# Performance work log

Hardware: AMD Instinct MI355X
Metric: run time of the kernel (lower is better)

## Reference

```python
import jax, jax.numpy as jnp
import numpy as np

N_USERS = 200000
N_ITEMS = 100000
N_NODES = N_USERS + N_ITEMS
EMBED_DIM = 64
N_LAYERS = 3
N_EDGES = 5000000
BATCH = 4096


def setup_inputs() -> dict:
    key = jax.random.key(0)
    ks = jax.random.split(key, 8)
    # Xavier-uniform-ish init for embedding tables
    lim = float(np.sqrt(6.0 / (N_USERS + EMBED_DIM)))
    user_emb = jax.random.uniform(ks[0], (N_USERS, EMBED_DIM), jnp.float32, -lim, lim)
    lim_i = float(np.sqrt(6.0 / (N_ITEMS + EMBED_DIM)))
    item_emb = jax.random.uniform(ks[1], (N_ITEMS, EMBED_DIM), jnp.float32, -lim_i, lim_i)
    # sparse normalized adjacency in COO form (values ~ 1/sqrt(du*di), use small positives)
    adj_vals = jax.random.uniform(ks[2], (N_EDGES,), jnp.float32, 0.0, 0.1)
    adj_rows = jax.random.randint(ks[3], (N_EDGES,), 0, N_NODES, jnp.int32)
    adj_cols = jax.random.randint(ks[4], (N_EDGES,), 0, N_NODES, jnp.int32)
    users = jax.random.randint(ks[5], (BATCH,), 0, N_USERS, jnp.int32)
    pos_items = jax.random.randint(ks[6], (BATCH,), 0, N_ITEMS, jnp.int32)
    neg_items = jax.random.randint(ks[7], (BATCH,), 0, N_ITEMS, jnp.int32)
    return {
        "user_emb": user_emb, "item_emb": item_emb, "adj_vals": adj_vals,
        "adj_rows": adj_rows, "adj_cols": adj_cols,
        "users": users, "pos_items": pos_items, "neg_items": neg_items,
    }


def _spmm(adj_rows, adj_cols, adj_vals, x):
    # y = A @ x for sparse COO A: gather source rows, scale, scatter-add to dest rows
    msgs = adj_vals[:, None] * x[adj_cols]          # [n_edges, d]
    return jax.ops.segment_sum(msgs, adj_rows, num_segments=N_NODES)


def reference(user_emb, item_emb, adj_vals, adj_rows, adj_cols, users, pos_items, neg_items):
    # E^0 = concat(user, item); E^k = A @ E^{k-1}; final = mean over k=0..K
    E = jnp.concatenate([user_emb, item_emb], axis=0)   # [N_NODES, d]
    acc = E
    cur = E
    for _ in range(N_LAYERS):
        cur = _spmm(adj_rows, adj_cols, adj_vals, cur)
        acc = acc + cur
    E_final = acc / jnp.asarray(N_LAYERS + 1, E.dtype)
    e_u = E_final[users]                         # users index into user block
    e_pos = E_final[N_USERS + pos_items]         # items offset by n_users
    e_neg = E_final[N_USERS + neg_items]
    return jnp.stack([e_u, e_pos, e_neg], axis=0)  # [3, B, d]
```

## Files before the change

kernel.cpp:

```cpp
#include <hip/hip_runtime.h>
#include <hip/hip_fp16.h>
#include <stdint.h>

#define N_USERS   200000
#define N_ITEMS   100000
#define N_NODES   300000
#define EMBED_DIM 64
#define N_EDGES   5000000
#define BATCH     4096

#define ROWS_PER_BUCKET 512
#define PART_K 586
#define PART_B 1024
#define CHUNK  ((N_EDGES + PART_B - 1) / PART_B)
#define PART_L (PART_K * PART_B)
#define SCAN_T 1024
#define SCAN_NB (PART_L / SCAN_T)

#define VAL_SCALE 81920.0f
#define VAL_INV   (1.0f / 81920.0f)
#define FIN_CAP   10240

__global__ void part_count(const int* __restrict__ rows, int* __restrict__ hist) {
    __shared__ int h[PART_K];
    for (int i = threadIdx.x; i < PART_K; i += blockDim.x) h[i] = 0;
    __syncthreads();
    int beg = blockIdx.x * CHUNK;
    int end = min(beg + CHUNK, N_EDGES);
    for (int i = beg + (int)threadIdx.x; i < end; i += blockDim.x)
        atomicAdd(&h[rows[i] >> 9], 1);
    __syncthreads();
    for (int i = threadIdx.x; i < PART_K; i += blockDim.x)
        hist[blockIdx.x * PART_K + i] = h[i];
}

__global__ void scan_partial(const int* __restrict__ hist,
                             int* __restrict__ local_scan,
                             int* __restrict__ block_sums) {
    __shared__ int sh[SCAN_T];
    int tid = threadIdx.x;
    int gid = blockIdx.x * SCAN_T + tid;
    int b = gid & (PART_B - 1);
    int k = gid >> 10;
    int v = hist[b * PART_K + k];
    sh[tid] = v;
    __syncthreads();
    for (int off = 1; off < SCAN_T; off <<= 1) {
        int t = (tid >= off) ? sh[tid - off] : 0;
        __syncthreads();
        sh[tid] += t;
        __syncthreads();
    }
    local_scan[gid] = sh[tid] - v;
    if (tid == SCAN_T - 1) block_sums[blockIdx.x] = sh[tid];
}

__global__ void scan_blocksums(int* __restrict__ block_sums) {
    __shared__ int sh[1024];
    int tid = threadIdx.x;
    int v = (tid < SCAN_NB) ? block_sums[tid] : 0;
    sh[tid] = v;
    __syncthreads();
    for (int off = 1; off < 1024; off <<= 1) {
        int t = (tid >= off) ? sh[tid - off] : 0;
        __syncthreads();
        sh[tid] += t;
        __syncthreads();
    }
    if (tid < SCAN_NB) block_sums[tid] = sh[tid] - v;
}

__global__ void scan_addoff(const int* __restrict__ local_scan,
                            const int* __restrict__ block_sums,
                            int* __restrict__ sofs,
                            int* __restrict__ row_ptr) {
    int gid = blockIdx.x * SCAN_T + threadIdx.x;
    sofs[gid] = local_scan[gid] + block_sums[blockIdx.x];
    if (gid == 0) row_ptr[N_NODES] = N_EDGES;
}

__global__ void part_scatter(const int* __restrict__ rows,
                             const int* __restrict__ cols,
                             const float* __restrict__ vals,
                             const int* __restrict__ sofs,
                             int2* __restrict__ part) {
    __shared__ int lcnt[PART_K];
    __shared__ int lbase[PART_K];
    __shared__ int gbase[PART_K];
    __shared__ int sc[1024];
    __shared__ int2 buf[CHUNK];
    __shared__ unsigned short bkt[CHUNK];
    int b = blockIdx.x;
    int tid = threadIdx.x;
    for (int i = tid; i < PART_K; i += 1024) {
        lcnt[i] = 0;
        gbase[i] = sofs[i * PART_B + b];
    }
    __syncthreads();
    int beg = b * CHUNK;
    int end = min(beg + CHUNK, N_EDGES);
    int n = end - beg;
    for (int i = beg + tid; i < end; i += 1024)
        atomicAdd(&lcnt[rows[i] >> 9], 1);
    __syncthreads();
    int v = (tid < PART_K) ? lcnt[tid] : 0;
    sc[tid] = v;
    __syncthreads();
    for (int off = 1; off < 1024; off <<= 1) {
        int t = (tid >= off) ? sc[tid - off] : 0;
        __syncthreads();
        sc[tid] += t;
        __syncthreads();
    }
    if (tid < PART_K) {
        int excl = sc[tid] - v;
        lbase[tid] = excl;
        lcnt[tid] = excl;
    }
    __syncthreads();
    for (int i = beg + tid; i < end; i += 1024) {
        int r = rows[i];
        int k = r >> 9;
        int p = atomicAdd(&lcnt[k], 1);
        buf[p] = make_int2(cols[i] | ((r & 511) << 19), __float_as_int(vals[i]));
        bkt[p] = (unsigned short)k;
    }
    __syncthreads();
    for (int i = tid; i < n; i += 1024) {
        int k = bkt[i];
        part[gbase[k] + (i - lbase[k])] = buf[i];
    }
}

__global__ void csr_finalize(const int2* __restrict__ part,
                             const int* __restrict__ sofs,
                             int* __restrict__ row_ptr,
                             unsigned int* __restrict__ sorted) {
    __shared__ int cnt[ROWS_PER_BUCKET];
    __shared__ int cur[ROWS_PER_BUCKET];
    __shared__ int sc[ROWS_PER_BUCKET];
    __shared__ unsigned int obuf[FIN_CAP];
    int k = blockIdx.x;
    int tid = threadIdx.x;
    int seg_beg = sofs[k * PART_B];
    int seg_end = (k + 1 < PART_K) ? sofs[(k + 1) * PART_B] : N_EDGES;
    int n = seg_end - seg_beg;

    cnt[tid] = 0;
    __syncthreads();
    for (int i = seg_beg + tid; i < seg_end; i += ROWS_PER_BUCKET)
        atomicAdd(&cnt[(part[i].x >> 19) & 511], 1);
    __syncthreads();

    int v = cnt[tid];
    sc[tid] = v;
    __syncthreads();
    for (int off = 1; off < 512; off <<= 1) {
        int t = (tid >= off) ? sc[tid - off] : 0;
        __syncthreads();
        sc[tid] += t;
        __syncthreads();
    }
    int excl = sc[tid] - v;

    int row = k * ROWS_PER_BUCKET + tid;
    if (row < N_NODES) row_ptr[row] = seg_beg + excl;
    cur[tid] = excl;
    __syncthreads();

    if (n <= FIN_CAP) {
        for (int i = seg_beg + tid; i < seg_end; i += ROWS_PER_BUCKET) {
            int2 p = part[i];
            int r = (p.x >> 19) & 511;
            int lp = atomicAdd(&cur[r], 1);
            float fv = __int_as_float(p.y);
            unsigned int q = (unsigned int)min(8191, (int)(fv * VAL_SCALE + 0.5f));
            obuf[lp] = (unsigned int)(p.x & 0x7FFFF) | (q << 19);
        }
        __syncthreads();
        for (int i = tid; i < n; i += ROWS_PER_BUCKET)
            sorted[seg_beg + i] = obuf[i];
    } else {
        for (int i = seg_beg + tid; i < seg_end; i += ROWS_PER_BUCKET) {
            int2 p = part[i];
            int r = (p.x >> 19) & 511;
            int lp = atomicAdd(&cur[r], 1);
            float fv = __int_as_float(p.y);
            unsigned int q = (unsigned int)min(8191, (int)(fv * VAL_SCALE + 0.5f));
            sorted[seg_beg + lp] = (unsigned int)(p.x & 0x7FFFF) | (q << 19);
        }
    }
}

__global__ void convert_emb(const float* __restrict__ ue,
                            const float* __restrict__ ie,
                            __half* __restrict__ xh) {
    int t = blockIdx.x * blockDim.x + threadIdx.x;
    if (t >= N_NODES * 16) return;
    int flat = t * 4;
    int row = flat >> 6;
    int off = flat & 63;
    const float* src = (row < N_USERS) ? (ue + (size_t)row * 64 + off)
                                       : (ie + (size_t)(row - N_USERS) * 64 + off);
    float4 v = *(const float4*)src;
    __half2 h0 = __floats2half2_rn(v.x, v.y);
    __half2 h1 = __floats2half2_rn(v.z, v.w);
    float2 packed;
    ((__half2*)&packed)[0] = h0;
    ((__half2*)&packed)[1] = h1;
    ((float2*)xh)[t] = packed;
}

#define ACC8(vv, r) { \
    const __half2* hp_ = (const __half2*)&(r); \
    float2 f0_ = __half22float2(hp_[0]); \
    float2 f1_ = __half22float2(hp_[1]); \
    float2 f2_ = __half22float2(hp_[2]); \
    float2 f3_ = __half22float2(hp_[3]); \
    acc[0] += (vv) * f0_.x; acc[1] += (vv) * f0_.y; \
    acc[2] += (vv) * f1_.x; acc[3] += (vv) * f1_.y; \
    acc[4] += (vv) * f2_.x; acc[5] += (vv) * f2_.y; \
    acc[6] += (vv) * f3_.x; acc[7] += (vv) * f3_.y; }

__global__ void spmm_h(const int* __restrict__ row_ptr,
                       const unsigned int* __restrict__ sorted,
                       const __half* __restrict__ xh,
                       __half* __restrict__ yh) {
    int t = blockIdx.x * blockDim.x + threadIdx.x;
    int row = t >> 3;
    int l8 = t & 7;
    if (row >= N_NODES) return;
    const float4* xv = (const float4*)xh;
    int beg = row_ptr[row];
    int end = row_ptr[row + 1];
    float acc[8] = {0.f, 0.f, 0.f, 0.f, 0.f, 0.f, 0.f, 0.f};
    int e = beg;
    for (; e + 2 <= end; e += 2) {
        unsigned int cv0 = sorted[e];
        unsigned int cv1 = sorted[e + 1];
        float4 r0 = xv[(size_t)(cv0 & 0x7FFFF) * 8 + l8];
        float4 r1 = xv[(size_t)(cv1 & 0x7FFFF) * 8 + l8];
        float v0 = (float)(cv0 >> 19) * VAL_INV;
        float v1 = (float)(cv1 >> 19) * VAL_INV;
        ACC8(v0, r0);
        ACC8(v1, r1);
    }
    if (e < end) {
        unsigned int cv = sorted[e];
        float4 r0 = xv[(size_t)(cv & 0x7FFFF) * 8 + l8];
        float v = (float)(cv >> 19) * VAL_INV;
        ACC8(v, r0);
    }
    float4 ov;
    ((__half2*)&ov)[0] = __floats2half2_rn(acc[0], acc[1]);
    ((__half2*)&ov)[1] = __floats2half2_rn(acc[2], acc[3]);
    ((__half2*)&ov)[2] = __floats2half2_rn(acc[4], acc[5]);
    ((__half2*)&ov)[3] = __floats2half2_rn(acc[6], acc[7]);
    ((float4*)yh)[(size_t)row * 8 + l8] = ov;
}

__global__ void final_kernel(const int* __restrict__ row_ptr,
                             const unsigned int* __restrict__ sorted,
                             const float* __restrict__ user_emb,
                             const float* __restrict__ item_emb,
                             const __half* __restrict__ E1h,
                             const __half* __restrict__ E2h,
                             const int* __restrict__ users,
                             const int* __restrict__ pos_items,
                             const int* __restrict__ neg_items,
                             float* __restrict__ out) {
    int t = blockIdx.x * blockDim.x + threadIdx.x;
    int slot = t >> 3;
    int l8 = t & 7;
    if (slot >= 3 * BATCH) return;
    int which = slot >> 12;
    int idx   = slot & (BATCH - 1);
    int node;
    if (which == 0)      node = users[idx];
    else if (which == 1) node = N_USERS + pos_items[idx];
    else                 node = N_USERS + neg_items[idx];

    const float4* e2v = (const float4*)E2h;

    float acc[8] = {0.f, 0.f, 0.f, 0.f, 0.f, 0.f, 0.f, 0.f};
    int beg = row_ptr[node];
    int end = row_ptr[node + 1];
    int e = beg;
    for (; e + 2 <= end; e += 2) {
        unsigned int cv0 = sorted[e];
        unsigned int cv1 = sorted[e + 1];
        float4 r0 = e2v[(size_t)(cv0 & 0x7FFFF) * 8 + l8];
        float4 r1 = e2v[(size_t)(cv1 & 0x7FFFF) * 8 + l8];
        float v0 = (float)(cv0 >> 19) * VAL_INV;
        float v1 = (float)(cv1 >> 19) * VAL_INV;
        ACC8(v0, r0);
        ACC8(v1, r1);
    }
    if (e < end) {
        unsigned int cv = sorted[e];
        float4 r0 = e2v[(size_t)(cv & 0x7FFFF) * 8 + l8];
        float v = (float)(cv >> 19) * VAL_INV;
        ACC8(v, r0);
    }

    const float* t0 = (node < N_USERS) ? (user_emb + (size_t)node * 64)
                                       : (item_emb + (size_t)(node - N_USERS) * 64);
    float4 e0a = ((const float4*)t0)[l8 * 2];
    float4 e0b = ((const float4*)t0)[l8 * 2 + 1];

    float4 e1c = ((const float4*)E1h)[(size_t)node * 8 + l8];
    float4 e2c = ((const float4*)E2h)[(size_t)node * 8 + l8];
    const __half2* h1 = (const __half2*)&e1c;
    const __half2* h2 = (const __half2*)&e2c;
    float e1[8], e2[8];
    {
        float2 a0 = __half22float2(h1[0]), a1 = __half22float2(h1[1]);
        float2 a2 = __half22float2(h1[2]), a3 = __half22float2(h1[3]);
        e1[0]=a0.x; e1[1]=a0.y; e1[2]=a1.x; e1[3]=a1.y;
        e1[4]=a2.x; e1[5]=a2.y; e1[6]=a3.x; e1[7]=a3.y;
        float2 b0 = __half22float2(h2[0]), b1 = __half22float2(h2[1]);
        float2 b2 = __half22float2(h2[2]), b3 = __half22float2(h2[3]);
        e2[0]=b0.x; e2[1]=b0.y; e2[2]=b1.x; e2[3]=b1.y;
        e2[4]=b2.x; e2[5]=b2.y; e2[6]=b3.x; e2[7]=b3.y;
    }
    float4 ra, rb;
    ra.x = (e0a.x + e1[0] + e2[0] + acc[0]) * 0.25f;
    ra.y = (e0a.y + e1[1] + e2[1] + acc[1]) * 0.25f;
    ra.z = (e0a.z + e1[2] + e2[2] + acc[2]) * 0.25f;
    ra.w = (e0a.w + e1[3] + e2[3] + acc[3]) * 0.25f;
    rb.x = (e0b.x + e1[4] + e2[4] + acc[4]) * 0.25f;
    rb.y = (e0b.y + e1[5] + e2[5] + acc[5]) * 0.25f;
    rb.z = (e0b.z + e1[6] + e2[6] + acc[6]) * 0.25f;
    rb.w = (e0b.w + e1[7] + e2[7] + acc[7]) * 0.25f;
    ((float4*)out)[(size_t)slot * 16 + l8 * 2]     = ra;
    ((float4*)out)[(size_t)slot * 16 + l8 * 2 + 1] = rb;
}

extern "C" void kernel_launch(void* const* d_in, const int* in_sizes, int n_in,
                              void* d_out, int out_size, void* d_ws, size_t ws_size,
                              hipStream_t stream) {
    const float* user_emb  = (const float*)d_in[0];
    const float* item_emb  = (const float*)d_in[1];
    const float* adj_vals  = (const float*)d_in[2];
    const int*   adj_rows  = (const int*)d_in[3];
    const int*   adj_cols  = (const int*)d_in[4];
    const int*   users     = (const int*)d_in[5];
    const int*   pos_items = (const int*)d_in[6];
    const int*   neg_items = (const int*)d_in[7];
    float* out = (float*)d_out;

    char* ws = (char*)d_ws;
    size_t off = 0;
    auto alloc = [&](size_t bytes) -> void* {
        void* p = ws + off;
        off = (off + bytes + 255) & ~(size_t)255;
        return p;
    };
    int*  hist       = (int*) alloc((size_t)(PART_L + 32) * sizeof(int));
    int*  local_scan = (int*) alloc((size_t)(PART_L + 32) * sizeof(int));
    int*  sofs       = (int*) alloc((size_t)(PART_L + 32) * sizeof(int));
    int*  block_sums = (int*) alloc((size_t)(SCAN_NB + 32) * sizeof(int));
    int*  row_ptr    = (int*) alloc((size_t)(N_NODES + 32) * sizeof(int));
    int2* part    = (int2*)alloc((size_t)N_EDGES * sizeof(int2));
    unsigned int* sorted = (unsigned int*)alloc((size_t)N_EDGES * sizeof(unsigned int));
    __half* x0h   = (__half*)alloc((size_t)N_NODES * EMBED_DIM * sizeof(__half));
    __half* E1h   = (__half*)alloc((size_t)N_NODES * EMBED_DIM * sizeof(__half));
    __half* E2h   = (__half*)alloc((size_t)N_NODES * EMBED_DIM * sizeof(__half));

    part_count<<<PART_B, 1024, 0, stream>>>(adj_rows, hist);
    scan_partial<<<SCAN_NB, SCAN_T, 0, stream>>>(hist, local_scan, block_sums);
    scan_blocksums<<<1, 1024, 0, stream>>>(block_sums);
    scan_addoff<<<SCAN_NB, SCAN_T, 0, stream>>>(local_scan, block_sums, sofs, row_ptr);
    part_scatter<<<PART_B, 1024, 0, stream>>>(adj_rows, adj_cols, adj_vals, sofs, part);
    csr_finalize<<<PART_K, ROWS_PER_BUCKET, 0, stream>>>(part, sofs, row_ptr, sorted);

    const int TB = 256;
    convert_emb<<<(N_NODES * 16 + TB - 1) / TB, TB, 0, stream>>>(user_emb, item_emb, x0h);

    int spmm_blocks = (N_NODES * 8 + TB - 1) / TB;
    spmm_h<<<spmm_blocks, TB, 0, stream>>>(row_ptr, sorted, x0h, E1h);
    spmm_h<<<spmm_blocks, TB, 0, stream>>>(row_ptr, sorted, E1h, E2h);

    int final_blocks = (3 * BATCH * 8 + TB - 1) / TB;
    final_kernel<<<final_blocks, TB, 0, stream>>>(
        row_ptr, sorted, user_emb, item_emb, E1h, E2h, users, pos_items, neg_items, out);
}
```

Baseline: 436.0 us.

## Vectorize partition loads, split payload/row arrays, swizzle chunk order, unroll SpMM by four

Edge-partition kernels now read rows, cols and vals as 128-bit vectors with a chunk size that is a multiple of four. Value quantization moves into the scatter kernel, and the 8-byte intermediate splits into a 4-byte payload plus a 2-byte local-row array, which cuts traffic into csr_finalize. Block-to-chunk order is swizzled in the scan and the scatter, changing which global offsets each block writes. The SpMM inner loop is unrolled to four gathers per iteration for more memory-level parallelism. The swizzle must stay consistent between part_count indexing and the scan mapping, or the CSR layout goes wrong.

```diff
diff --git a/kernel.cpp b/kernel.cpp
--- a/kernel.cpp
+++ b/kernel.cpp
@@ -12,7 +12,7 @@
 #define ROWS_PER_BUCKET 512
 #define PART_K 586
 #define PART_B 1024
-#define CHUNK  ((N_EDGES + PART_B - 1) / PART_B)
+#define CHUNK  4884
 #define PART_L (PART_K * PART_B)
 #define SCAN_T 1024
 #define SCAN_NB (PART_L / SCAN_T)
@@ -21,14 +21,21 @@
 #define VAL_INV   (1.0f / 81920.0f)
 #define FIN_CAP   10240
 
+__device__ __forceinline__ int swz(int b)     { return ((b & 7) << 7) | (b >> 3); }
+
 __global__ void part_count(const int* __restrict__ rows, int* __restrict__ hist) {
     __shared__ int h[PART_K];
     for (int i = threadIdx.x; i < PART_K; i += blockDim.x) h[i] = 0;
     __syncthreads();
     int beg = blockIdx.x * CHUNK;
     int end = min(beg + CHUNK, N_EDGES);
-    for (int i = beg + (int)threadIdx.x; i < end; i += blockDim.x)
-        atomicAdd(&h[rows[i] >> 9], 1);
+    for (int i = beg + (int)threadIdx.x * 4; i < end; i += blockDim.x * 4) {
+        int4 r4 = *(const int4*)(rows + i);
+        atomicAdd(&h[r4.x >> 9], 1);
+        atomicAdd(&h[r4.y >> 9], 1);
+        atomicAdd(&h[r4.z >> 9], 1);
+        atomicAdd(&h[r4.w >> 9], 1);
+    }
     __syncthreads();
     for (int i = threadIdx.x; i < PART_K; i += blockDim.x)
         hist[blockIdx.x * PART_K + i] = h[i];
@@ -40,8 +47,9 @@
     __shared__ int sh[SCAN_T];
     int tid = threadIdx.x;
     int gid = blockIdx.x * SCAN_T + tid;
-    int b = gid & (PART_B - 1);
+    int p = gid & (PART_B - 1);
     int k = gid >> 10;
+    int b = ((p & 127) << 3) | (p >> 7);
     int v = hist[b * PART_K + k];
     sh[tid] = v;
     __syncthreads();
@@ -83,25 +91,33 @@
                              const int* __restrict__ cols,
                              const float* __restrict__ vals,
                              const int* __restrict__ sofs,
-                             int2* __restrict__ part) {
+                             unsigned int* __restrict__ ppay,
+                             unsigned short* __restrict__ prloc) {
     __shared__ int lcnt[PART_K];
     __shared__ int lbase[PART_K];
     __shared__ int gbase[PART_K];
     __shared__ int sc[1024];
-    __shared__ int2 buf[CHUNK];
-    __shared__ unsigned short bkt[CHUNK];
+    __shared__ unsigned int   pay[CHUNK];
+    __shared__ unsigned short rl[CHUNK];
+    __shared__ unsigned short bk[CHUNK];
     int b = blockIdx.x;
     int tid = threadIdx.x;
+    int myp = swz(b);
     for (int i = tid; i < PART_K; i += 1024) {
         lcnt[i] = 0;
-        gbase[i] = sofs[i * PART_B + b];
+        gbase[i] = sofs[i * PART_B + myp];
     }
     __syncthreads();
     int beg = b * CHUNK;
     int end = min(beg + CHUNK, N_EDGES);
     int n = end - beg;
-    for (int i = beg + tid; i < end; i += 1024)
-        atomicAdd(&lcnt[rows[i] >> 9], 1);
+    for (int i = beg + tid * 4; i < end; i += 4096) {
+        int4 r4 = *(const int4*)(rows + i);
+        atomicAdd(&lcnt[r4.x >> 9], 1);
+        atomicAdd(&lcnt[r4.y >> 9], 1);
+        atomicAdd(&lcnt[r4.z >> 9], 1);
+        atomicAdd(&lcnt[r4.w >> 9], 1);
+    }
     __syncthreads();
     int v = (tid < PART_K) ? lcnt[tid] : 0;
     sc[tid] = v;
@@ -118,21 +134,35 @@
         lcnt[tid] = excl;
     }
     __syncthreads();
-    for (int i = beg + tid; i < end; i += 1024) {
-        int r = rows[i];
-        int k = r >> 9;
-        int p = atomicAdd(&lcnt[k], 1);
-        buf[p] = make_int2(cols[i] | ((r & 511) << 19), __float_as_int(vals[i]));
-        bkt[p] = (unsigned short)k;
+    for (int i = beg + tid * 4; i < end; i += 4096) {
+        int4 r4 = *(const int4*)(rows + i);
+        int4 c4 = *(const int4*)(cols + i);
+        float4 v4 = *(const float4*)(vals + i);
+        int rr[4] = {r4.x, r4.y, r4.z, r4.w};
+        int cc[4] = {c4.x, c4.y, c4.z, c4.w};
+        float vv[4] = {v4.x, v4.y, v4.z, v4.w};
+        #pragma unroll
+        for (int j = 0; j < 4; ++j) {
+            int r = rr[j];
+            int k = r >> 9;
+            int p = atomicAdd(&lcnt[k], 1);
+            unsigned int q = (unsigned int)min(8191, (int)(vv[j] * VAL_SCALE + 0.5f));
+            pay[p] = (unsigned int)cc[j] | (q << 19);
+            rl[p] = (unsigned short)(r & 511);
+            bk[p] = (unsigned short)k;
+        }
     }
     __syncthreads();
     for (int i = tid; i < n; i += 1024) {
-        int k = bkt[i];
-        part[gbase[k] + (i - lbase[k])] = buf[i];
-    }
-}
-
-__global__ void csr_finalize(const int2* __restrict__ part,
+        int k = bk[i];
+        int a = gbase[k] + (i - lbase[k]);
+        ppay[a] = pay[i];
+        prloc[a] = rl[i];
+    }
+}
+
+__global__ void csr_finalize(const unsigned int* __restrict__ ppay,
+                             const unsigned short* __restrict__ prloc,
                              const int* __restrict__ sofs,
                              int* __restrict__ row_ptr,
                              unsigned int* __restrict__ sorted) {
@@ -149,7 +179,7 @@
     cnt[tid] = 0;
     __syncthreads();
     for (int i = seg_beg + tid; i < seg_end; i += ROWS_PER_BUCKET)
-        atomicAdd(&cnt[(part[i].x >> 19) & 511], 1);
+        atomicAdd(&cnt[prloc[i]], 1);
     __syncthreads();
 
     int v = cnt[tid];
@@ -170,24 +200,18 @@
 
     if (n <= FIN_CAP) {
         for (int i = seg_beg + tid; i < seg_end; i += ROWS_PER_BUCKET) {
-            int2 p = part[i];
-            int r = (p.x >> 19) & 511;
+            int r = prloc[i];
             int lp = atomicAdd(&cur[r], 1);
-            float fv = __int_as_float(p.y);
-            unsigned int q = (unsigned int)min(8191, (int)(fv * VAL_SCALE + 0.5f));
-            obuf[lp] = (unsigned int)(p.x & 0x7FFFF) | (q << 19);
+            obuf[lp] = ppay[i];
         }
         __syncthreads();
         for (int i = tid; i < n; i += ROWS_PER_BUCKET)
             sorted[seg_beg + i] = obuf[i];
     } else {
         for (int i = seg_beg + tid; i < seg_end; i += ROWS_PER_BUCKET) {
-            int2 p = part[i];
-            int r = (p.x >> 19) & 511;
+            int r = prloc[i];
             int lp = atomicAdd(&cur[r], 1);
-            float fv = __int_as_float(p.y);
-            unsigned int q = (unsigned int)min(8191, (int)(fv * VAL_SCALE + 0.5f));
-            sorted[seg_beg + lp] = (unsigned int)(p.x & 0x7FFFF) | (q << 19);
+            sorted[seg_beg + lp] = ppay[i];
         }
     }
 }
@@ -235,17 +259,25 @@
     int end = row_ptr[row + 1];
     float acc[8] = {0.f, 0.f, 0.f, 0.f, 0.f, 0.f, 0.f, 0.f};
     int e = beg;
-    for (; e + 2 <= end; e += 2) {
+    for (; e + 4 <= end; e += 4) {
         unsigned int cv0 = sorted[e];
         unsigned int cv1 = sorted[e + 1];
+        unsigned int cv2 = sorted[e + 2];
+        unsigned int cv3 = sorted[e + 3];
         float4 r0 = xv[(size_t)(cv0 & 0x7FFFF) * 8 + l8];
         float4 r1 = xv[(size_t)(cv1 & 0x7FFFF) * 8 + l8];
+        float4 r2 = xv[(size_t)(cv2 & 0x7FFFF) * 8 + l8];
+        float4 r3 = xv[(size_t)(cv3 & 0x7FFFF) * 8 + l8];
         float v0 = (float)(cv0 >> 19) * VAL_INV;
         float v1 = (float)(cv1 >> 19) * VAL_INV;
+        float v2 = (float)(cv2 >> 19) * VAL_INV;
+        float v3 = (float)(cv3 >> 19) * VAL_INV;
         ACC8(v0, r0);
         ACC8(v1, r1);
-    }
-    if (e < end) {
+        ACC8(v2, r2);
+        ACC8(v3, r3);
+    }
+    for (; e < end; ++e) {
         unsigned int cv = sorted[e];
         float4 r0 = xv[(size_t)(cv & 0x7FFFF) * 8 + l8];
         float v = (float)(cv >> 19) * VAL_INV;
@@ -361,7 +393,8 @@
     int*  sofs       = (int*) alloc((size_t)(PART_L + 32) * sizeof(int));
     int*  block_sums = (int*) alloc((size_t)(SCAN_NB + 32) * sizeof(int));
     int*  row_ptr    = (int*) alloc((size_t)(N_NODES + 32) * sizeof(int));
-    int2* part    = (int2*)alloc((size_t)N_EDGES * sizeof(int2));
+    unsigned int*   ppay  = (unsigned int*)  alloc((size_t)N_EDGES * sizeof(unsigned int));
+    unsigned short* prloc = (unsigned short*)alloc((size_t)N_EDGES * sizeof(unsigned short));
     unsigned int* sorted = (unsigned int*)alloc((size_t)N_EDGES * sizeof(unsigned int));
     __half* x0h   = (__half*)alloc((size_t)N_NODES * EMBED_DIM * sizeof(__half));
     __half* E1h   = (__half*)alloc((size_t)N_NODES * EMBED_DIM * sizeof(__half));
@@ -371,8 +404,8 @@
     scan_partial<<<SCAN_NB, SCAN_T, 0, stream>>>(hist, local_scan, block_sums);
     scan_blocksums<<<1, 1024, 0, stream>>>(block_sums);
     scan_addoff<<<SCAN_NB, SCAN_T, 0, stream>>>(local_scan, block_sums, sofs, row_ptr);
-    part_scatter<<<PART_B, 1024, 0, stream>>>(adj_rows, adj_cols, adj_vals, sofs, part);
-    csr_finalize<<<PART_K, ROWS_PER_BUCKET, 0, stream>>>(part, sofs, row_ptr, sorted);
+    part_scatter<<<PART_B, 1024, 0, stream>>>(adj_rows, adj_cols, adj_vals, sofs, ppay, prloc);
+    csr_finalize<<<PART_K, ROWS_PER_BUCKET, 0, stream>>>(ppay, prloc, sofs, row_ptr, sorted);
 
     const int TB = 256;
     convert_emb<<<(N_NODES * 16 + TB - 1) / TB, TB, 0, stream>>>(user_emb, item_emb, x0h);
```

Result: faster. 422.7 us (-3.0%).
